# Optimization experiments

Measured on AMD Instinct MI355X. Metric: run time of the kernel, lower is better.

Reference implementation:

```python
import jax, jax.numpy as jnp
import numpy as np

TEMPERATURE = 0.07
EPS = 1e-8
B, D, C = 4096, 512, 10


def setup_inputs() -> dict:
    key = jax.random.key(0)
    k1, k2 = jax.random.split(key)
    features = jax.random.normal(k1, (B, D), dtype=jnp.float32)
    cls = jax.random.randint(k2, (B,), 0, C)
    labels = jax.nn.one_hot(cls, C, dtype=jnp.float32)  # [B, C] one-hot
    return {"features": features, "labels": labels}


def reference(features, labels):
    b = features.shape[0]
    # L2-normalize rows
    feats = features / jnp.linalg.norm(features, axis=1, keepdims=True)
    sim = jnp.clip(feats @ feats.T / TEMPERATURE, -20.0, 20.0)  # [B, B]
    eye = jnp.eye(b, dtype=bool)
    sim = jnp.where(eye, -jnp.inf, sim)  # mask self-similarity

    labels_norm = labels / (labels.sum(axis=1, keepdims=True) + EPS)
    label_sim = labels_norm @ labels_norm.T  # [B, B]
    label_sim = jnp.where(eye, 0.0, label_sim)
    pos_mask = label_sim > 0.1  # [B, B] bool

    exp_sim = jnp.exp(sim)  # diag -> exp(-inf) = 0
    pos_sum = jnp.sum(jnp.where(pos_mask, exp_sim, 0.0), axis=1)  # [B]
    all_sum = jnp.sum(exp_sim, axis=1)  # diag already zero => off-diagonal sum
    loss_i = -jnp.log(pos_sum / (all_sum + EPS) + EPS)  # [B]

    valid = jnp.any(pos_mask, axis=1)  # rows with >=1 positive
    n_valid = jnp.sum(valid.astype(jnp.float32))
    total = jnp.sum(jnp.where(valid, loss_i, 0.0))
    return jnp.where(n_valid > 0, total / n_valid, 0.0)
```

## Files before the change

### kernel.cpp

```cpp
#include <hip/hip_runtime.h>


#define B_ROWS 4096
#define D_DIM  512
#define C_CLS  10
#define NT     64
#define NTILES (NT * (NT + 1) / 2)

typedef float f32x4 __attribute__((ext_vector_type(4)));

__device__ __forceinline__ void load_lds16(const void* g, void* l) {
  __builtin_amdgcn_global_load_lds(
      (const __attribute__((address_space(1))) unsigned int*)g,
      (__attribute__((address_space(3))) unsigned int*)l, 16, 0, 0);
}

__global__ __launch_bounds__(256) void prep_kernel(
    const float* __restrict__ feats, const float* __restrict__ labels,
    unsigned char* __restrict__ F8, int* __restrict__ cls,
    float* __restrict__ out) {
  const int w = threadIdx.x >> 6, lane = threadIdx.x & 63;
  const int row = blockIdx.x * 4 + w;
  const float* fr = feats + (size_t)row * D_DIM;
  float4 v0 = ((const float4*)fr)[2 * lane];
  float4 v1 = ((const float4*)fr)[2 * lane + 1];
  float ss = v0.x*v0.x + v0.y*v0.y + v0.z*v0.z + v0.w*v0.w
           + v1.x*v1.x + v1.y*v1.y + v1.z*v1.z + v1.w*v1.w;
  #pragma unroll
  for (int m = 1; m < 64; m <<= 1) ss += __shfl_xor(ss, m, 64);
  float inv = 1.0f / sqrtf(ss);

  int p0 = __builtin_amdgcn_cvt_pk_fp8_f32(v0.x * inv, v0.y * inv, 0, 0);
  p0     = __builtin_amdgcn_cvt_pk_fp8_f32(v0.z * inv, v0.w * inv, p0, 1);
  int p1 = __builtin_amdgcn_cvt_pk_fp8_f32(v1.x * inv, v1.y * inv, 0, 0);
  p1     = __builtin_amdgcn_cvt_pk_fp8_f32(v1.z * inv, v1.w * inv, p1, 1);
  int2 pk; pk.x = p0; pk.y = p1;
  *(int2*)(F8 + (size_t)row * D_DIM + 8 * lane) = pk;

  float lv = (lane < C_CLS) ? labels[(size_t)row * C_CLS + lane] : 0.f;
  unsigned long long m = __ballot(lv > 0.5f);
  if (lane == 0) cls[row] = (int)(__ffsll((long long)m) - 1);
  if (blockIdx.x == 0 && threadIdx.x == 0) out[0] = 0.f;
}

__global__ __launch_bounds__(256, 8) void sim_kernel(
    const unsigned char* __restrict__ F8, const int* __restrict__ cls,
    float* __restrict__ P_all, float* __restrict__ P_pos) {
  __shared__ __align__(16) unsigned char Abuf[64 * 128];
  __shared__ __align__(16) unsigned char Bbuf[64 * 128];
  __shared__ int clsA[64], clsB[64];
  __shared__ float g_row_all[64], g_row_pos[64];
  __shared__ float g_col_all[64], g_col_pos[64];

  int rem = blockIdx.x, bi = 0, rowlen = NT;
  while (rem >= rowlen) { rem -= rowlen; ++bi; --rowlen; }
  const int bj = bi + rem;
  const int i0 = bi * 64, j0 = bj * 64;
  const bool offdiag = (bi != bj);

  const int t = threadIdx.x;
  const int w = t >> 6;
  const int lane = t & 63;
  const int q = lane >> 4;
  const int cl = lane & 15;

  if (t < 64) { clsA[t] = cls[i0 + t]; g_col_all[t] = 0.f; g_col_pos[t] = 0.f; }
  else if (t < 128) clsB[t - 64] = cls[j0 + t - 64];

  f32x4 acc[4];
  #pragma unroll
  for (int c = 0; c < 4; ++c) acc[c] = (f32x4){0.f, 0.f, 0.f, 0.f};

  const int srow = lane >> 3;
  const int sg   = (lane & 7) ^ srow;

  for (int k0 = 0; k0 < D_DIM; k0 += 128) {
    __syncthreads();
    #pragma unroll
    for (int r = 0; r < 2; ++r) {
      const int rowbase = 16 * w + r * 8;
      load_lds16(F8 + (size_t)(i0 + rowbase + srow) * D_DIM + k0 + sg * 16,
                 &Abuf[rowbase * 128]);
      load_lds16(F8 + (size_t)(j0 + rowbase + srow) * D_DIM + k0 + sg * 16,
                 &Bbuf[rowbase * 128]);
    }
    __syncthreads();

    #pragma unroll
    for (int ks = 0; ks < 4; ++ks) {
      const int g = ks * 2 + (q >> 1);
      const int h = (q & 1) * 8;
      const int ar = 16 * w + cl;
      long af = *(const long*)&Abuf[ar * 128 + ((g ^ (ar & 7)) * 16) + h];
      long bf[4];
      #pragma unroll
      for (int c = 0; c < 4; ++c) {
        const int br = 16 * c + cl;
        bf[c] = *(const long*)&Bbuf[br * 128 + ((g ^ (br & 7)) * 16) + h];
      }
      #pragma unroll
      for (int c = 0; c < 4; ++c)
        acc[c] = __builtin_amdgcn_mfma_f32_16x16x32_fp8_fp8(
            af, bf[c], acc[c], 0, 0, 0);
    }
  }

  const float invT = 1.0f / 0.07f;
  float sum_all[4] = {0.f, 0.f, 0.f, 0.f};
  float sum_pos[4] = {0.f, 0.f, 0.f, 0.f};
  float cs_all[4]  = {0.f, 0.f, 0.f, 0.f};
  float cs_pos[4]  = {0.f, 0.f, 0.f, 0.f};

  #pragma unroll
  for (int c = 0; c < 4; ++c) {
    const int jloc = 16*c + cl;
    const int gj = j0 + jloc;
    const int cj = clsB[jloc];
    #pragma unroll
    for (int r = 0; r < 4; ++r) {
      const int iloc = 16*w + q*4 + r;
      const int gi = i0 + iloc;
      float s = acc[c][r] * invT;
      s = fminf(fmaxf(s, -20.f), 20.f);
      const bool diag = (gi == gj);
      float e = diag ? 0.f : __expf(s);
      sum_all[r] += e;
      cs_all[c] += e;
      if (!diag && cj == clsA[iloc]) { sum_pos[r] += e; cs_pos[c] += e; }
    }
  }

  #pragma unroll
  for (int r = 0; r < 4; ++r) {
    float sa = sum_all[r], sp = sum_pos[r];
    #pragma unroll
    for (int m = 1; m < 16; m <<= 1) {
      sa += __shfl_xor(sa, m, 64);
      sp += __shfl_xor(sp, m, 64);
    }
    if (cl == 0) {
      const int rloc = 16*w + q*4 + r;
      g_row_all[rloc] = sa;
      g_row_pos[rloc] = sp;
    }
  }

  if (offdiag) {
    #pragma unroll
    for (int c = 0; c < 4; ++c) {
      float sa = cs_all[c], sp = cs_pos[c];
      sa += __shfl_xor(sa, 16, 64); sa += __shfl_xor(sa, 32, 64);
      sp += __shfl_xor(sp, 16, 64); sp += __shfl_xor(sp, 32, 64);
      if (q == 0) {
        atomicAdd(&g_col_all[16*c + cl], sa);
        atomicAdd(&g_col_pos[16*c + cl], sp);
      }
    }
  }
  __syncthreads();

  if (w == 0) {
    const size_t base_row = ((size_t)bi * 64 + bj) * 64;
    P_all[base_row + lane] = g_row_all[lane];
    P_pos[base_row + lane] = g_row_pos[lane];
  } else if (w == 1 && offdiag) {
    const size_t base_col = ((size_t)bj * 64 + bi) * 64;
    P_all[base_col + lane] = g_col_all[lane];
    P_pos[base_col + lane] = g_col_pos[lane];
  }
}

__global__ __launch_bounds__(256) void finalize_kernel(
    const float* __restrict__ P_all, const float* __restrict__ P_pos,
    float* __restrict__ out) {
  __shared__ float Sall[4096], Spos[4096];
  const int s = blockIdx.x;
  const int t = threadIdx.x;
  for (int i = t; i < 4096; i += 256) {
    Sall[i] = P_all[(size_t)s * 4096 + i];
    Spos[i] = P_pos[(size_t)s * 4096 + i];
  }
  __syncthreads();
  if (t < 64) {
    float a = 0.f, p = 0.f;
    #pragma unroll 8
    for (int k = 0; k < 64; ++k) {
      a += Sall[k * 64 + t];
      p += Spos[k * 64 + t];
    }
    float loss = 0.f;
    if (p > 0.f)
      loss = -logf(p / (a + 1e-8f) + 1e-8f);
    #pragma unroll
    for (int m = 1; m < 64; m <<= 1) loss += __shfl_xor(loss, m, 64);
    if (t == 0)
      atomicAdd(&out[0], loss * (1.0f / (float)B_ROWS));
  }
}

extern "C" void kernel_launch(void* const* d_in, const int* in_sizes, int n_in,
                              void* d_out, int out_size, void* d_ws, size_t ws_size,
                              hipStream_t stream) {
  const float* features = (const float*)d_in[0];
  const float* labels   = (const float*)d_in[1];
  float* out = (float*)d_out;

  unsigned char* F8 = (unsigned char*)d_ws;
  int*   cls   = (int*)((char*)d_ws + (size_t)B_ROWS * D_DIM);
  float* P_all = (float*)((char*)cls + B_ROWS * sizeof(int));
  float* P_pos = P_all + (size_t)NT * NT * 64;

  prep_kernel<<<B_ROWS / 4, 256, 0, stream>>>(features, labels, F8, cls, out);
  sim_kernel<<<NTILES, 256, 0, stream>>>(F8, cls, P_all, P_pos);
  finalize_kernel<<<NT, 256, 0, stream>>>(P_all, P_pos, out);
}
```

Before: 89.90 us.

## Process two adjacent upper-triangle tiles per block sharing the A row-panel

```diff
diff --git a/kernel.cpp b/kernel.cpp
--- a/kernel.cpp
+++ b/kernel.cpp
@@ -5,7 +5,7 @@
 #define D_DIM  512
 #define C_CLS  10
 #define NT     64
-#define NTILES (NT * (NT + 1) / 2)
+#define NPAIR  1056
 
 typedef float f32x4 __attribute__((ext_vector_type(4)));
 
@@ -43,130 +43,169 @@
   if (blockIdx.x == 0 && threadIdx.x == 0) out[0] = 0.f;
 }
 
-__global__ __launch_bounds__(256, 8) void sim_kernel(
+__global__ __launch_bounds__(256, 4) void sim_kernel(
     const unsigned char* __restrict__ F8, const int* __restrict__ cls,
     float* __restrict__ P_all, float* __restrict__ P_pos) {
-  __shared__ __align__(16) unsigned char Abuf[64 * 128];
-  __shared__ __align__(16) unsigned char Bbuf[64 * 128];
-  __shared__ int clsA[64], clsB[64];
-  __shared__ float g_row_all[64], g_row_pos[64];
-  __shared__ float g_col_all[64], g_col_pos[64];
-
-  int rem = blockIdx.x, bi = 0, rowlen = NT;
-  while (rem >= rowlen) { rem -= rowlen; ++bi; --rowlen; }
-  const int bj = bi + rem;
-  const int i0 = bi * 64, j0 = bj * 64;
-  const bool offdiag = (bi != bj);
+  __shared__ __align__(16) unsigned char Abuf [64 * 128];
+  __shared__ __align__(16) unsigned char B0buf[64 * 128];
+  __shared__ __align__(16) unsigned char B1buf[64 * 128];
+  __shared__ int clsA[64], clsB[2][64];
+  __shared__ float g_row_all[2][64], g_row_pos[2][64];
+  __shared__ float g_col_all[2][64], g_col_pos[2][64];
+
+  int rem = blockIdx.x, bi = 0, rl = (NT + 1) >> 1;
+  while (rem >= rl) { rem -= rl; ++bi; rl = (NT - bi + 1) >> 1; }
+  const int bj0 = bi + 2 * rem;
+  const int bj1 = bj0 + 1;
+  const bool has2 = (bj1 < NT);
+  const bool diag0 = (bj0 == bi);
+  const int i0 = bi * 64, j0a = bj0 * 64, j0b = bj1 * 64;
 
   const int t = threadIdx.x;
-  const int w = t >> 6;
-  const int lane = t & 63;
-  const int q = lane >> 4;
-  const int cl = lane & 15;
-
-  if (t < 64) { clsA[t] = cls[i0 + t]; g_col_all[t] = 0.f; g_col_pos[t] = 0.f; }
-  else if (t < 128) clsB[t - 64] = cls[j0 + t - 64];
-
-  f32x4 acc[4];
+  const int w = t >> 6, lane = t & 63;
+  const int ti = w >> 1;
+  const int ws = w & 1;
+  const int q = lane >> 4, cl = lane & 15;
+  const bool live = (ti == 0) || has2;
+
+  if (t < 64)        clsA[t] = cls[i0 + t];
+  else if (t < 128)  clsB[0][t - 64] = cls[j0a + t - 64];
+  else if (t < 192) { if (has2) clsB[1][t - 128] = cls[j0b + t - 128]; }
+  if (t < 128) { g_col_all[t >> 6][t & 63] = 0.f; g_col_pos[t >> 6][t & 63] = 0.f; }
+
+  f32x4 acc[2][4];
   #pragma unroll
-  for (int c = 0; c < 4; ++c) acc[c] = (f32x4){0.f, 0.f, 0.f, 0.f};
+  for (int ri = 0; ri < 2; ++ri)
+    #pragma unroll
+    for (int c = 0; c < 4; ++c) acc[ri][c] = (f32x4){0.f, 0.f, 0.f, 0.f};
 
   const int srow = lane >> 3;
   const int sg   = (lane & 7) ^ srow;
+  const unsigned char* Bp = (ti == 0) ? (diag0 ? Abuf : B0buf) : B1buf;
 
   for (int k0 = 0; k0 < D_DIM; k0 += 128) {
     __syncthreads();
     #pragma unroll
-    for (int r = 0; r < 2; ++r) {
-      const int rowbase = 16 * w + r * 8;
-      load_lds16(F8 + (size_t)(i0 + rowbase + srow) * D_DIM + k0 + sg * 16,
-                 &Abuf[rowbase * 128]);
-      load_lds16(F8 + (size_t)(j0 + rowbase + srow) * D_DIM + k0 + sg * 16,
-                 &Bbuf[rowbase * 128]);
+    for (int j = 0; j < 6; ++j) {
+      const int s  = 6 * w + j;
+      const int op = s >> 3;
+      const int rb = (s & 7) * 8;
+      if (op == 0) {
+        load_lds16(F8 + (size_t)(i0 + rb + srow) * D_DIM + k0 + sg * 16,
+                   &Abuf[rb * 128]);
+      } else if (op == 1) {
+        if (!diag0)
+          load_lds16(F8 + (size_t)(j0a + rb + srow) * D_DIM + k0 + sg * 16,
+                     &B0buf[rb * 128]);
+      } else {
+        if (has2)
+          load_lds16(F8 + (size_t)(j0b + rb + srow) * D_DIM + k0 + sg * 16,
+                     &B1buf[rb * 128]);
+      }
     }
     __syncthreads();
 
-    #pragma unroll
-    for (int ks = 0; ks < 4; ++ks) {
-      const int g = ks * 2 + (q >> 1);
-      const int h = (q & 1) * 8;
-      const int ar = 16 * w + cl;
-      long af = *(const long*)&Abuf[ar * 128 + ((g ^ (ar & 7)) * 16) + h];
-      long bf[4];
+    if (live) {
+      #pragma unroll
+      for (int ks = 0; ks < 4; ++ks) {
+        const int g = ks * 2 + (q >> 1);
+        const int h = (q & 1) * 8;
+        long af[2], bf[4];
+        #pragma unroll
+        for (int ri = 0; ri < 2; ++ri) {
+          const int ar = 32 * ws + 16 * ri + cl;
+          af[ri] = *(const long*)&Abuf[ar * 128 + ((g ^ (ar & 7)) * 16) + h];
+        }
+        #pragma unroll
+        for (int c = 0; c < 4; ++c) {
+          const int br = 16 * c + cl;
+          bf[c] = *(const long*)&Bp[br * 128 + ((g ^ (br & 7)) * 16) + h];
+        }
+        #pragma unroll
+        for (int ri = 0; ri < 2; ++ri)
+          #pragma unroll
+          for (int c = 0; c < 4; ++c)
+            acc[ri][c] = __builtin_amdgcn_mfma_f32_16x16x32_fp8_fp8(
+                af[ri], bf[c], acc[ri][c], 0, 0, 0);
+      }
+    }
+  }
+
+  if (live) {
+    const float invT = 1.0f / 0.07f;
+    const int jbase = (ti == 0) ? j0a : j0b;
+    const bool tdiag = (ti == 0) && diag0;
+    float cs_all[4] = {0.f, 0.f, 0.f, 0.f};
+    float cs_pos[4] = {0.f, 0.f, 0.f, 0.f};
+
+    #pragma unroll
+    for (int ri = 0; ri < 2; ++ri) {
+      float sum_all[4] = {0.f, 0.f, 0.f, 0.f};
+      float sum_pos[4] = {0.f, 0.f, 0.f, 0.f};
       #pragma unroll
       for (int c = 0; c < 4; ++c) {
-        const int br = 16 * c + cl;
-        bf[c] = *(const long*)&Bbuf[br * 128 + ((g ^ (br & 7)) * 16) + h];
-      }
-      #pragma unroll
-      for (int c = 0; c < 4; ++c)
-        acc[c] = __builtin_amdgcn_mfma_f32_16x16x32_fp8_fp8(
-            af, bf[c], acc[c], 0, 0, 0);
-    }
-  }
-
-  const float invT = 1.0f / 0.07f;
-  float sum_all[4] = {0.f, 0.f, 0.f, 0.f};
-  float sum_pos[4] = {0.f, 0.f, 0.f, 0.f};
-  float cs_all[4]  = {0.f, 0.f, 0.f, 0.f};
-  float cs_pos[4]  = {0.f, 0.f, 0.f, 0.f};
-
-  #pragma unroll
-  for (int c = 0; c < 4; ++c) {
-    const int jloc = 16*c + cl;
-    const int gj = j0 + jloc;
-    const int cj = clsB[jloc];
-    #pragma unroll
-    for (int r = 0; r < 4; ++r) {
-      const int iloc = 16*w + q*4 + r;
-      const int gi = i0 + iloc;
-      float s = acc[c][r] * invT;
-      s = fminf(fmaxf(s, -20.f), 20.f);
-      const bool diag = (gi == gj);
-      float e = diag ? 0.f : __expf(s);
-      sum_all[r] += e;
-      cs_all[c] += e;
-      if (!diag && cj == clsA[iloc]) { sum_pos[r] += e; cs_pos[c] += e; }
-    }
-  }
-
-  #pragma unroll
-  for (int r = 0; r < 4; ++r) {
-    float sa = sum_all[r], sp = sum_pos[r];
-    #pragma unroll
-    for (int m = 1; m < 16; m <<= 1) {
-      sa += __shfl_xor(sa, m, 64);
-      sp += __shfl_xor(sp, m, 64);
-    }
-    if (cl == 0) {
-      const int rloc = 16*w + q*4 + r;
-      g_row_all[rloc] = sa;
-      g_row_pos[rloc] = sp;
-    }
-  }
-
-  if (offdiag) {
-    #pragma unroll
-    for (int c = 0; c < 4; ++c) {
-      float sa = cs_all[c], sp = cs_pos[c];
-      sa += __shfl_xor(sa, 16, 64); sa += __shfl_xor(sa, 32, 64);
-      sp += __shfl_xor(sp, 16, 64); sp += __shfl_xor(sp, 32, 64);
-      if (q == 0) {
-        atomicAdd(&g_col_all[16*c + cl], sa);
-        atomicAdd(&g_col_pos[16*c + cl], sp);
+        const int jloc = 16*c + cl;
+        const int gj = jbase + jloc;
+        const int cj = clsB[ti][jloc];
+        #pragma unroll
+        for (int r = 0; r < 4; ++r) {
+          const int iloc = 32*ws + 16*ri + q*4 + r;
+          const int gi = i0 + iloc;
+          float s = acc[ri][c][r] * invT;
+          s = fminf(fmaxf(s, -20.f), 20.f);
+          const bool diag = (gi == gj);
+          float e = diag ? 0.f : __expf(s);
+          sum_all[r] += e;
+          cs_all[c] += e;
+          if (!diag && cj == clsA[iloc]) { sum_pos[r] += e; cs_pos[c] += e; }
+        }
+      }
+      #pragma unroll
+      for (int r = 0; r < 4; ++r) {
+        float sa = sum_all[r], sp = sum_pos[r];
+        #pragma unroll
+        for (int m = 1; m < 16; m <<= 1) {
+          sa += __shfl_xor(sa, m, 64);
+          sp += __shfl_xor(sp, m, 64);
+        }
+        if (cl == 0) {
+          const int rloc = 32*ws + 16*ri + q*4 + r;
+          g_row_all[ti][rloc] = sa;
+          g_row_pos[ti][rloc] = sp;
+        }
+      }
+    }
+    if (!tdiag) {
+      #pragma unroll
+      for (int c = 0; c < 4; ++c) {
+        float sa = cs_all[c], sp = cs_pos[c];
+        sa += __shfl_xor(sa, 16, 64); sa += __shfl_xor(sa, 32, 64);
+        sp += __shfl_xor(sp, 16, 64); sp += __shfl_xor(sp, 32, 64);
+        if (q == 0) {
+          atomicAdd(&g_col_all[ti][16*c + cl], sa);
+          atomicAdd(&g_col_pos[ti][16*c + cl], sp);
+        }
       }
     }
   }
   __syncthreads();
 
   if (w == 0) {
-    const size_t base_row = ((size_t)bi * 64 + bj) * 64;
-    P_all[base_row + lane] = g_row_all[lane];
-    P_pos[base_row + lane] = g_row_pos[lane];
-  } else if (w == 1 && offdiag) {
-    const size_t base_col = ((size_t)bj * 64 + bi) * 64;
-    P_all[base_col + lane] = g_col_all[lane];
-    P_pos[base_col + lane] = g_col_pos[lane];
+    const size_t b = ((size_t)bi * NT + bj0) * 64;
+    P_all[b + lane] = g_row_all[0][lane];
+    P_pos[b + lane] = g_row_pos[0][lane];
+  } else if (w == 1 && !diag0) {
+    const size_t b = ((size_t)bj0 * NT + bi) * 64;
+    P_all[b + lane] = g_col_all[0][lane];
+    P_pos[b + lane] = g_col_pos[0][lane];
+  } else if (w == 2 && has2) {
+    const size_t b = ((size_t)bi * NT + bj1) * 64;
+    P_all[b + lane] = g_row_all[1][lane];
+    P_pos[b + lane] = g_row_pos[1][lane];
+  } else if (w == 3 && has2) {
+    const size_t b = ((size_t)bj1 * NT + bi) * 64;
+    P_all[b + lane] = g_col_all[1][lane];
+    P_pos[b + lane] = g_col_pos[1][lane];
   }
 }
 
@@ -211,6 +250,6 @@
   float* P_pos = P_all + (size_t)NT * NT * 64;
 
   prep_kernel<<<B_ROWS / 4, 256, 0, stream>>>(features, labels, F8, cls, out);
-  sim_kernel<<<NTILES, 256, 0, stream>>>(F8, cls, P_all, P_pos);
+  sim_kernel<<<NPAIR, 256, 0, stream>>>(F8, cls, P_all, P_pos);
   finalize_kernel<<<NT, 256, 0, stream>>>(P_all, P_pos, out);
 }
```

After: 88.04 us. -2.1%, faster.

## Double-buffer LDS tiles and use 2 waves each computing 32 rows

Applied to the files above, without the earlier changes.

```diff
diff --git a/kernel.cpp b/kernel.cpp
--- a/kernel.cpp
+++ b/kernel.cpp
@@ -43,11 +43,11 @@
   if (blockIdx.x == 0 && threadIdx.x == 0) out[0] = 0.f;
 }
 
-__global__ __launch_bounds__(256, 8) void sim_kernel(
+__global__ __launch_bounds__(128) void sim_kernel(
     const unsigned char* __restrict__ F8, const int* __restrict__ cls,
     float* __restrict__ P_all, float* __restrict__ P_pos) {
-  __shared__ __align__(16) unsigned char Abuf[64 * 128];
-  __shared__ __align__(16) unsigned char Bbuf[64 * 128];
+  __shared__ __align__(16) unsigned char Abuf[2][64 * 128];
+  __shared__ __align__(16) unsigned char Bbuf[2][64 * 128];
   __shared__ int clsA[64], clsB[64];
   __shared__ float g_row_all[64], g_row_pos[64];
   __shared__ float g_col_all[64], g_col_pos[64];
@@ -65,83 +65,100 @@
   const int cl = lane & 15;
 
   if (t < 64) { clsA[t] = cls[i0 + t]; g_col_all[t] = 0.f; g_col_pos[t] = 0.f; }
-  else if (t < 128) clsB[t - 64] = cls[j0 + t - 64];
-
-  f32x4 acc[4];
-  #pragma unroll
-  for (int c = 0; c < 4; ++c) acc[c] = (f32x4){0.f, 0.f, 0.f, 0.f};
+  else        clsB[t - 64] = cls[j0 + t - 64];
+
+  f32x4 acc[2][4];
+  #pragma unroll
+  for (int ri = 0; ri < 2; ++ri)
+    #pragma unroll
+    for (int c = 0; c < 4; ++c) acc[ri][c] = (f32x4){0.f, 0.f, 0.f, 0.f};
 
   const int srow = lane >> 3;
   const int sg   = (lane & 7) ^ srow;
 
-  for (int k0 = 0; k0 < D_DIM; k0 += 128) {
+  #define STAGE(k0, b)                                                        \
+    _Pragma("unroll")                                                         \
+    for (int r = 0; r < 4; ++r) {                                             \
+      const int rowbase = 32 * w + r * 8;        \
+      load_lds16(F8 + (size_t)(i0 + rowbase + srow) * D_DIM + (k0) + sg * 16, \
+                 &Abuf[b][rowbase * 128]);                                    \
+      load_lds16(F8 + (size_t)(j0 + rowbase + srow) * D_DIM + (k0) + sg * 16, \
+                 &Bbuf[b][rowbase * 128]);                                    \
+    }
+
+  STAGE(0, 0)
+
+  #pragma unroll
+  for (int it = 0; it < 4; ++it) {
     __syncthreads();
-    #pragma unroll
-    for (int r = 0; r < 2; ++r) {
-      const int rowbase = 16 * w + r * 8;
-      load_lds16(F8 + (size_t)(i0 + rowbase + srow) * D_DIM + k0 + sg * 16,
-                 &Abuf[rowbase * 128]);
-      load_lds16(F8 + (size_t)(j0 + rowbase + srow) * D_DIM + k0 + sg * 16,
-                 &Bbuf[rowbase * 128]);
-    }
-    __syncthreads();
+    if (it < 3) { STAGE((it + 1) * 128, (it + 1) & 1) }
+    const unsigned char* Ab = &Abuf[it & 1][0];
+    const unsigned char* Bb = &Bbuf[it & 1][0];
 
     #pragma unroll
     for (int ks = 0; ks < 4; ++ks) {
       const int g = ks * 2 + (q >> 1);
       const int h = (q & 1) * 8;
-      const int ar = 16 * w + cl;
-      long af = *(const long*)&Abuf[ar * 128 + ((g ^ (ar & 7)) * 16) + h];
-      long bf[4];
+      long af[2], bf[4];
+      #pragma unroll
+      for (int ri = 0; ri < 2; ++ri) {
+        const int ar = 32 * w + 16 * ri + cl;
+        af[ri] = *(const long*)&Ab[ar * 128 + ((g ^ (ar & 7)) * 16) + h];
+      }
       #pragma unroll
       for (int c = 0; c < 4; ++c) {
         const int br = 16 * c + cl;
-        bf[c] = *(const long*)&Bbuf[br * 128 + ((g ^ (br & 7)) * 16) + h];
-      }
-      #pragma unroll
-      for (int c = 0; c < 4; ++c)
-        acc[c] = __builtin_amdgcn_mfma_f32_16x16x32_fp8_fp8(
-            af, bf[c], acc[c], 0, 0, 0);
-    }
-  }
+        bf[c] = *(const long*)&Bb[br * 128 + ((g ^ (br & 7)) * 16) + h];
+      }
+      #pragma unroll
+      for (int ri = 0; ri < 2; ++ri)
+        #pragma unroll
+        for (int c = 0; c < 4; ++c)
+          acc[ri][c] = __builtin_amdgcn_mfma_f32_16x16x32_fp8_fp8(
+              af[ri], bf[c], acc[ri][c], 0, 0, 0);
+    }
+  }
+  #undef STAGE
 
   const float invT = 1.0f / 0.07f;
-  float sum_all[4] = {0.f, 0.f, 0.f, 0.f};
-  float sum_pos[4] = {0.f, 0.f, 0.f, 0.f};
-  float cs_all[4]  = {0.f, 0.f, 0.f, 0.f};
-  float cs_pos[4]  = {0.f, 0.f, 0.f, 0.f};
-
-  #pragma unroll
-  for (int c = 0; c < 4; ++c) {
-    const int jloc = 16*c + cl;
-    const int gj = j0 + jloc;
-    const int cj = clsB[jloc];
+  float cs_all[4] = {0.f, 0.f, 0.f, 0.f};
+  float cs_pos[4] = {0.f, 0.f, 0.f, 0.f};
+
+  #pragma unroll
+  for (int ri = 0; ri < 2; ++ri) {
+    float sum_all[4] = {0.f, 0.f, 0.f, 0.f};
+    float sum_pos[4] = {0.f, 0.f, 0.f, 0.f};
+    #pragma unroll
+    for (int c = 0; c < 4; ++c) {
+      const int jloc = 16*c + cl;
+      const int gj = j0 + jloc;
+      const int cj = clsB[jloc];
+      #pragma unroll
+      for (int r = 0; r < 4; ++r) {
+        const int iloc = 32*w + 16*ri + q*4 + r;
+        const int gi = i0 + iloc;
+        float s = acc[ri][c][r] * invT;
+        s = fminf(fmaxf(s, -20.f), 20.f);
+        const bool diag = (gi == gj);
+        float e = diag ? 0.f : __expf(s);
+        sum_all[r] += e;
+        cs_all[c] += e;
+        if (!diag && cj == clsA[iloc]) { sum_pos[r] += e; cs_pos[c] += e; }
+      }
+    }
     #pragma unroll
     for (int r = 0; r < 4; ++r) {
-      const int iloc = 16*w + q*4 + r;
-      const int gi = i0 + iloc;
-      float s = acc[c][r] * invT;
-      s = fminf(fmaxf(s, -20.f), 20.f);
-      const bool diag = (gi == gj);
-      float e = diag ? 0.f : __expf(s);
-      sum_all[r] += e;
-      cs_all[c] += e;
-      if (!diag && cj == clsA[iloc]) { sum_pos[r] += e; cs_pos[c] += e; }
-    }
-  }
-
-  #pragma unroll
-  for (int r = 0; r < 4; ++r) {
-    float sa = sum_all[r], sp = sum_pos[r];
-    #pragma unroll
-    for (int m = 1; m < 16; m <<= 1) {
-      sa += __shfl_xor(sa, m, 64);
-      sp += __shfl_xor(sp, m, 64);
-    }
-    if (cl == 0) {
-      const int rloc = 16*w + q*4 + r;
-      g_row_all[rloc] = sa;
-      g_row_pos[rloc] = sp;
+      float sa = sum_all[r], sp = sum_pos[r];
+      #pragma unroll
+      for (int m = 1; m < 16; m <<= 1) {
+        sa += __shfl_xor(sa, m, 64);
+        sp += __shfl_xor(sp, m, 64);
+      }
+      if (cl == 0) {
+        const int rloc = 32*w + 16*ri + q*4 + r;
+        g_row_all[rloc] = sa;
+        g_row_pos[rloc] = sp;
+      }
     }
   }
 
@@ -163,7 +180,7 @@
     const size_t base_row = ((size_t)bi * 64 + bj) * 64;
     P_all[base_row + lane] = g_row_all[lane];
     P_pos[base_row + lane] = g_row_pos[lane];
-  } else if (w == 1 && offdiag) {
+  } else if (offdiag) {
     const size_t base_col = ((size_t)bj * 64 + bi) * 64;
     P_all[base_col + lane] = g_col_all[lane];
     P_pos[base_col + lane] = g_col_pos[lane];
@@ -211,6 +228,6 @@
   float* P_pos = P_all + (size_t)NT * NT * 64;
 
   prep_kernel<<<B_ROWS / 4, 256, 0, stream>>>(features, labels, F8, cls, out);
-  sim_kernel<<<NTILES, 256, 0, stream>>>(F8, cls, P_all, P_pos);
+  sim_kernel<<<NTILES, 128, 0, stream>>>(F8, cls, P_all, P_pos);
   finalize_kernel<<<NT, 256, 0, stream>>>(P_all, P_pos, out);
 }
```

Result: no change. 89.45 us (-0.5%).
